# Kernel tuning notes

Hardware: AMD Instinct MI355X
Metric: run time of the kernel (lower is better)

The kernel has to match this reference:

```python
import jax, jax.numpy as jnp
import numpy as np

N = 100000
E = 1600000
EMB = 256
D = 128
B = 4096
L = 50
NCLASS = 10


def _spmm(edge_src, edge_dst, edge_w, h):
    # adj @ h with adj given as weighted edge list (dst aggregates from src)
    msg = h[edge_src] * edge_w[:, None]          # [E, D]
    return jax.ops.segment_sum(msg, edge_dst, num_segments=h.shape[0])


def setup_inputs() -> dict:
    key = jax.random.key(0)
    ks = jax.random.split(key, 20)
    inp = {}
    inp["A1_tensor"] = jax.random.normal(ks[0], (N, EMB), dtype=jnp.float32)
    inp["edge_src"] = jax.random.randint(ks[1], (E,), 0, N, dtype=jnp.int32)
    inp["edge_dst"] = jax.random.randint(ks[2], (E,), 0, N, dtype=jnp.int32)
    inp["edge_w"] = jax.random.uniform(ks[3], (E,), dtype=jnp.float32)
    inp["batch_idx"] = jax.random.randint(ks[4], (B, 1, L), 0, N, dtype=jnp.int32)
    s = 0.05  # modest init scale for numerical sanity
    inp["w_gc1"] = jax.random.normal(ks[5], (EMB, D), dtype=jnp.float32) * s
    inp["b_gc1"] = jax.random.normal(ks[6], (D,), dtype=jnp.float32) * s
    inp["w_gc2"] = jax.random.normal(ks[7], (D, D), dtype=jnp.float32) * s
    inp["b_gc2"] = jax.random.normal(ks[8], (D,), dtype=jnp.float32) * s
    inp["n_param"] = jax.random.uniform(ks[9], (N, 1), dtype=jnp.float32)
    inp["Lin1"] = jax.random.normal(ks[10], (EMB, D), dtype=jnp.float32) * s
    inp["Lin1_bias"] = jax.random.normal(ks[11], (D,), dtype=jnp.float32) * s
    inp["weight2"] = jax.random.normal(ks[12], (D, 64), dtype=jnp.float32) * s
    inp["bias2"] = jax.random.normal(ks[13], (64,), dtype=jnp.float32) * s
    inp["lin1_w"] = jax.random.normal(ks[14], ((L + 1) * 64, D), dtype=jnp.float32) * s
    inp["lin1_b"] = jax.random.normal(ks[15], (D,), dtype=jnp.float32) * s
    inp["classifier"] = jax.random.normal(ks[16], (D, NCLASS), dtype=jnp.float32) * s
    inp["classifier_bias"] = jax.random.normal(ks[17], (NCLASS,), dtype=jnp.float32) * s
    return inp


def reference(A1_tensor, edge_src, edge_dst, edge_w, batch_idx,
              w_gc1, b_gc1, w_gc2, b_gc2, n_param, Lin1, Lin1_bias,
              weight2, bias2, lin1_w, lin1_b, classifier, classifier_bias):
    # eval mode: both dropouts are identity
    a0 = A1_tensor @ Lin1 + Lin1_bias              # [N, D]
    a1 = a0 * n_param                              # per-node convex gate
    x1 = _spmm(edge_src, edge_dst, edge_w, A1_tensor @ w_gc1 + b_gc1)  # gc1
    x1 = a1 + x1 * (1.0 - n_param)
    x2 = _spmm(edge_src, edge_dst, edge_w, x1 @ w_gc2 + b_gc2)         # gc2
    bidx = batch_idx[:, 0, :]                      # [B, L]
    sel = x2[bidx]                                 # [B, L, D] irregular gather
    sel = jnp.concatenate([sel, jnp.sum(sel, axis=1, keepdims=True)], axis=1)  # [B, L+1, D]
    sel = jnp.einsum('bld,de->ble', sel, weight2) + bias2                      # [B, L+1, 64]
    sel = sel.reshape(bidx.shape[0], -1)           # [B, (L+1)*64]
    sel = sel @ lin1_w + lin1_b                    # [B, D]
    pre = sel @ classifier + classifier_bias       # [B, nclass]
    return (jnp.argmax(pre, axis=-1), sel)
```

## Files before the change

### kernel.cpp

```cpp
#include <hip/hip_runtime.h>
#include <cstdint>

#define NN   100000
#define EE   1600000
#define EMBD 256
#define DD   128
#define BBB  4096
#define LLL  50
#define NCLS 10

#define NB   196
#define BSH  9
#define EPB  4096

#define FIXS 1048576.0f
#define INVS (1.0f / 1048576.0f)

typedef __attribute__((ext_vector_type(8))) short bf16x8;
typedef __attribute__((ext_vector_type(4))) float f32x4;

__device__ __forceinline__ ushort f2bf(float f) {
  uint32_t u = __float_as_uint(f);
  u += 0x7fffu + ((u >> 16) & 1u);
  return (ushort)(u >> 16);
}
__device__ __forceinline__ float bf2f(ushort h) {
  return __uint_as_float(((uint32_t)h) << 16);
}

template<int BM, int BN, int BK, int TM, int TN>
__global__ __launch_bounds__(256)
void gemm_f32(const float* __restrict__ Av, int lda,
              const float* __restrict__ W, int ldw,
              const float* __restrict__ bias,
              float* __restrict__ Cv, int ldc,
              int M, int ktot, int kper,
              const int* __restrict__ bidxg,
              const float* __restrict__ Sg)
{
  constexpr int TX = BN / TN;
  constexpr int TY = BM / TM;
  static_assert(TX * TY == 256, "thread mapping");
  static_assert(TN % 4 == 0, "epilogue uses 4-wide vectors");
  constexpr int AQ = BK / 4;
  constexpr int ALOADS = (BM * AQ) / 256;
  static_assert((BM * AQ) % 256 == 0, "A-tile load mapping");
  constexpr int WQ4 = BN / 4;
  constexpr int WLOADS = (BK * WQ4) / 256;
  static_assert((BK * WQ4) % 256 == 0, "W-tile load mapping");

  __shared__ float As[BK][BM + 4];
  __shared__ float Ws[BK][BN];

  const int tid = threadIdx.x;
  const int tx = tid % TX, ty = tid / TX;
  const int bm0 = blockIdx.x * BM;
  const int bn0 = blockIdx.y * BN;
  const int z = blockIdx.z;
  const int koff = z * kper;
  int kc = ktot - koff; if (kc > kper) kc = kper;
  W += bn0 + (size_t)koff * ldw;
  Cv += (size_t)z * (size_t)M * ldc;
  const float* biasp = bias ? bias + bn0 : nullptr;

  float acc[TM][TN];
#pragma unroll
  for (int i = 0; i < TM; ++i)
#pragma unroll
    for (int j = 0; j < TN; ++j) acc[i][j] = 0.f;

  for (int kt = 0; kt < kc; kt += BK) {
#pragma unroll
    for (int p = 0; p < ALOADS; ++p) {
      int f = tid + p * 256;
      int row = f / AQ, q = f % AQ;
      int arow = bm0 + row;
      float4 av = make_float4(0.f, 0.f, 0.f, 0.f);
      if (arow < M) {
        if (bidxg) {
          int k = koff + kt + (q << 2);
          int l = k >> 6, jj = k & 63;
          const float* ap = (l < LLL)
              ? (Av + (size_t)bidxg[arow * LLL + l] * 64 + jj)
              : (Sg + (size_t)arow * 64 + jj);
          av = *(const float4*)ap;
        } else {
          av = *(const float4*)(Av + (long long)arow * lda + koff + kt + (q << 2));
        }
      }
      As[(q << 2) + 0][row] = av.x;
      As[(q << 2) + 1][row] = av.y;
      As[(q << 2) + 2][row] = av.z;
      As[(q << 2) + 3][row] = av.w;
    }
#pragma unroll
    for (int p = 0; p < WLOADS; ++p) {
      int f = tid + p * 256;
      int krow = f / WQ4, c4 = f % WQ4;
      *(float4*)&Ws[krow][c4 << 2] =
          *(const float4*)(W + (long long)(kt + krow) * ldw + (c4 << 2));
    }
    __syncthreads();
#pragma unroll
    for (int kk = 0; kk < BK; ++kk) {
      float a[TM], b[TN];
      if constexpr (TM % 4 == 0) {
#pragma unroll
        for (int i = 0; i < TM; i += 4)
          *(float4*)&a[i] = *(const float4*)&As[kk][ty * TM + i];
      } else {
#pragma unroll
        for (int i = 0; i < TM; ++i) a[i] = As[kk][ty * TM + i];
      }
#pragma unroll
      for (int j = 0; j < TN; j += 4)
        *(float4*)&b[j] = *(const float4*)&Ws[kk][tx * TN + j];
#pragma unroll
      for (int i = 0; i < TM; ++i)
#pragma unroll
        for (int j = 0; j < TN; ++j)
          acc[i][j] = fmaf(a[i], b[j], acc[i][j]);
    }
    __syncthreads();
  }

#pragma unroll
  for (int i = 0; i < TM; ++i) {
    int r = bm0 + ty * TM + i;
    if (r >= M) continue;
#pragma unroll
    for (int j4 = 0; j4 < TN; j4 += 4) {
      float4 v = make_float4(acc[i][j4], acc[i][j4 + 1],
                             acc[i][j4 + 2], acc[i][j4 + 3]);
      if (biasp != nullptr) {
        v.x += biasp[tx * TN + j4 + 0]; v.y += biasp[tx * TN + j4 + 1];
        v.z += biasp[tx * TN + j4 + 2]; v.w += biasp[tx * TN + j4 + 3];
      }
      *(float4*)(Cv + (long long)r * ldc + bn0 + tx * TN + j4) = v;
    }
  }
}

__global__ __launch_bounds__(256)
void gemm_qp_mfma(const float* __restrict__ A1,
                  const ushort* __restrict__ Wfh,
                  const ushort* __restrict__ Wfl,
                  const float* __restrict__ bab,
                  float* __restrict__ Qb, float* __restrict__ Pb, int M)
{
  __shared__ ushort LAh[128][40];
  __shared__ ushort LAl[128][40];
  const int tid = threadIdx.x;
  const int w = tid >> 6, l = tid & 63;
  const int bm0 = blockIdx.x * 128;
  const int srow = tid >> 1;
  const int skh = (tid & 1) << 4;
  const int fk = (l >> 4) << 3;

  f32x4 acc[2][8];
#pragma unroll
  for (int rt = 0; rt < 2; ++rt)
#pragma unroll
    for (int c = 0; c < 8; ++c) acc[rt][c] = (f32x4){0.f, 0.f, 0.f, 0.f};

  for (int kt8 = 0; kt8 < 8; ++kt8) {
    {
      int grow = bm0 + srow;
      float x[16];
      if (grow < M) {
        const float* ap = A1 + (size_t)grow * 256 + (kt8 << 5) + skh;
        *(float4*)&x[0]  = *(const float4*)ap;
        *(float4*)&x[4]  = *(const float4*)(ap + 4);
        *(float4*)&x[8]  = *(const float4*)(ap + 8);
        *(float4*)&x[12] = *(const float4*)(ap + 12);
      } else {
#pragma unroll
        for (int j = 0; j < 16; ++j) x[j] = 0.f;
      }
      ushort h[16], lo[16];
#pragma unroll
      for (int j = 0; j < 16; ++j) {
        h[j] = f2bf(x[j]);
        lo[j] = f2bf(x[j] - bf2f(h[j]));
      }
      *(bf16x8*)&LAh[srow][skh]     = *(bf16x8*)&h[0];
      *(bf16x8*)&LAh[srow][skh + 8] = *(bf16x8*)&h[8];
      *(bf16x8*)&LAl[srow][skh]     = *(bf16x8*)&lo[0];
      *(bf16x8*)&LAl[srow][skh + 8] = *(bf16x8*)&lo[8];
    }
    __syncthreads();

    bf16x8 ah[2], al[2];
#pragma unroll
    for (int rt = 0; rt < 2; ++rt) {
      int frow = (w << 5) + (rt << 4) + (l & 15);
      ah[rt] = *(const bf16x8*)&LAh[frow][fk];
      al[rt] = *(const bf16x8*)&LAl[frow][fk];
    }
#pragma unroll
    for (int ct = 0; ct < 8; ++ct) {
      size_t off = ((size_t)((kt8 << 3) + ct) * 64 + l) << 3;
      bf16x8 bh = *(const bf16x8*)(Wfh + off);
      bf16x8 bl = *(const bf16x8*)(Wfl + off);
#pragma unroll
      for (int rt = 0; rt < 2; ++rt) {
        acc[rt][ct] = __builtin_amdgcn_mfma_f32_16x16x32_bf16(ah[rt], bh, acc[rt][ct], 0, 0, 0);
        acc[rt][ct] = __builtin_amdgcn_mfma_f32_16x16x32_bf16(ah[rt], bl, acc[rt][ct], 0, 0, 0);
        acc[rt][ct] = __builtin_amdgcn_mfma_f32_16x16x32_bf16(al[rt], bh, acc[rt][ct], 0, 0, 0);
      }
    }
    __syncthreads();
  }

#pragma unroll
  for (int rt = 0; rt < 2; ++rt) {
    const int r0 = bm0 + (w << 5) + (rt << 4) + ((l >> 4) << 2);
#pragma unroll
    for (int ct = 0; ct < 8; ++ct) {
      int gcol = (ct << 4) + (l & 15);
      float bia = bab[gcol];
      float* dst = (gcol < 64) ? (Qb + gcol) : (Pb + (gcol - 64));
#pragma unroll
      for (int r = 0; r < 4; ++r) {
        int grow = r0 + r;
        if (grow < M) dst[(size_t)grow * 64] = acc[rt][ct][r] + bia;
      }
    }
  }
}

__global__ __launch_bounds__(256)
void wfrag_k(const float* __restrict__ Wab, ushort* __restrict__ Wfh,
             ushort* __restrict__ Wfl)
{
  int t = blockIdx.x * 256 + threadIdx.x;
  if (t >= 4096) return;
  int f = t >> 6, l = t & 63;
  int kt = f >> 3, ct = f & 7;
  int row0 = (kt << 5) + ((l >> 4) << 3);
  int col = (ct << 4) + (l & 15);
  ushort h[8], lo[8];
#pragma unroll
  for (int j = 0; j < 8; ++j) {
    float x = Wab[(row0 + j) * 128 + col];
    h[j] = f2bf(x);
    lo[j] = f2bf(x - bf2f(h[j]));
  }
  size_t off = ((size_t)t) << 3;
  *(bf16x8*)(Wfh + off) = *(bf16x8*)h;
  *(bf16x8*)(Wfl + off) = *(bf16x8*)lo;
}

__global__ __launch_bounds__(256)
void fuse1_k(const float* __restrict__ wgc1, const float* __restrict__ lin1,
             const float* __restrict__ bgc1, const float* __restrict__ lin1b,
             const float* __restrict__ wgc2,
             float* __restrict__ T1, float* __restrict__ T2,
             float* __restrict__ ta, float* __restrict__ tb)
{
  int t = blockIdx.x * 256 + threadIdx.x;
  const float* Arow; float* outp; int n;
  if (t < 32768)      { n = t & 127; Arow = wgc1 + (t >> 7) * 128; outp = T1 + t; }
  else if (t < 65536) { int u = t - 32768; n = u & 127; Arow = lin1 + (u >> 7) * 128; outp = T2 + u; }
  else if (t < 65664) { n = t - 65536; Arow = bgc1;  outp = ta + n; }
  else if (t < 65792) { n = t - 65664; Arow = lin1b; outp = tb + n; }
  else return;
  float s = 0.f;
  for (int k = 0; k < 128; ++k) s = fmaf(Arow[k], wgc2[k * 128 + n], s);
  *outp = s;
}

__global__ __launch_bounds__(256)
void fuse2_k(const float* __restrict__ T1, const float* __restrict__ T2,
             const float* __restrict__ ta, const float* __restrict__ tb,
             const float* __restrict__ bgc2, const float* __restrict__ w2,
             float* __restrict__ Wab, float* __restrict__ bab,
             float* __restrict__ bcv)
{
  int t = blockIdx.x * 256 + threadIdx.x;
  const float* Arow; float* outp; int j;
  if (t < 32768) {
    int c = t & 127; j = c & 63;
    Arow = (c < 64 ? T1 : T2) + (t >> 7) * 128;
    outp = Wab + t;
  } else if (t < 32896) {
    int c = t - 32768; j = c & 63; Arow = (c < 64) ? ta : tb; outp = bab + c;
  } else if (t < 32960) {
    j = t - 32896; Arow = bgc2; outp = bcv + j;
  } else return;
  float s = 0.f;
  for (int k = 0; k < 128; ++k) s = fmaf(Arow[k], w2[k * 64 + j], s);
  *outp = s;
}

__global__ __launch_bounds__(256)
void cnt_k(const int* __restrict__ edst, int* __restrict__ gbkt)
{
  __shared__ int l[NB];
  const int tid = threadIdx.x;
  for (int i = tid; i < NB; i += 256) l[i] = 0;
  __syncthreads();
  const int e0 = blockIdx.x * EPB;
  const int e1 = min(EE, e0 + EPB);
#pragma unroll
  for (int u = 0; u < 16; ++u) {
    int e = e0 + u * 256 + tid;
    if (e < e1) atomicAdd(&l[edst[e] >> BSH], 1);
  }
  __syncthreads();
  for (int i = tid; i < NB; i += 256)
    if (l[i]) atomicAdd(&gbkt[i], l[i]);
}

__global__ __launch_bounds__(256)
void scanB_k(const int* __restrict__ gbkt, int* __restrict__ bbase,
             int* __restrict__ gcur, int* __restrict__ rp)
{
  __shared__ int s[256];
  int t = threadIdx.x;
  int v = (t < NB) ? gbkt[t] : 0;
  s[t] = v;
  __syncthreads();
  for (int off = 1; off < 256; off <<= 1) {
    int u = (t >= off) ? s[t - off] : 0;
    __syncthreads();
    s[t] += u;
    __syncthreads();
  }
  if (t < NB) {
    int ex = s[t] - v;
    bbase[t] = ex;
    gcur[t] = ex;
  }
  if (t == 0) { bbase[NB] = EE; rp[NN] = EE; }
}

__global__ __launch_bounds__(256)
void bin_k(const int* __restrict__ edst, const int* __restrict__ esrc,
           const float* __restrict__ ew, int* __restrict__ gcur,
           int4* __restrict__ ebd)
{
  __shared__ int lcnt[NB];
  __shared__ int lbase[NB];
  const int tid = threadIdx.x;
  const int e0 = blockIdx.x * EPB;
  const int e1 = min(EE, e0 + EPB);
  for (int i = tid; i < NB; i += 256) lcnt[i] = 0;
  __syncthreads();
  int dv[16], sv[16], wv[16];
#pragma unroll
  for (int u = 0; u < 16; ++u) {
    int e = e0 + u * 256 + tid;
    if (e < e1) {
      dv[u] = edst[e];
      sv[u] = esrc[e];
      wv[u] = __float_as_int(ew[e]);
      atomicAdd(&lcnt[dv[u] >> BSH], 1);
    } else dv[u] = -1;
  }
  __syncthreads();
  for (int i = tid; i < NB; i += 256) {
    lbase[i] = atomicAdd(&gcur[i], lcnt[i]);
    lcnt[i] = 0;
  }
  __syncthreads();
#pragma unroll
  for (int u = 0; u < 16; ++u) {
    if (dv[u] >= 0) {
      int c = dv[u] >> BSH;
      int k = atomicAdd(&lcnt[c], 1);
      int4 p; p.x = dv[u]; p.y = sv[u]; p.z = wv[u]; p.w = 0;
      ebd[lbase[c] + k] = p;
    }
  }
}

__global__ __launch_bounds__(256)
void sort_k(const int4* __restrict__ ebd, const int* __restrict__ bbase,
            int* __restrict__ rp, int2* __restrict__ sw)
{
  __shared__ int hist[512];
  __shared__ int excl[512];
  __shared__ int s2[256];
  __shared__ int lcur[512];
  const int c = blockIdx.x;
  const int n0 = c << BSH;
  const int n1 = min(NN, n0 + 512);
  const int nn = n1 - n0;
  const int tid = threadIdx.x;
  for (int i = tid; i < 512; i += 256) { hist[i] = 0; lcur[i] = 0; }
  __syncthreads();
  const int b0 = bbase[c];
  const int b1 = bbase[c + 1];
  for (int i = b0 + tid; i < b1; i += 256)
    atomicAdd(&hist[ebd[i].x - n0], 1);
  __syncthreads();
  int a0 = hist[2 * tid], a1 = hist[2 * tid + 1];
  s2[tid] = a0 + a1;
  __syncthreads();
  for (int off = 1; off < 256; off <<= 1) {
    int u = (tid >= off) ? s2[tid - off] : 0;
    __syncthreads();
    s2[tid] += u;
    __syncthreads();
  }
  int pe = tid ? s2[tid - 1] : 0;
  excl[2 * tid] = pe;
  excl[2 * tid + 1] = pe + a0;
  if (2 * tid < nn)     rp[n0 + 2 * tid]     = b0 + pe;
  if (2 * tid + 1 < nn) rp[n0 + 2 * tid + 1] = b0 + pe + a0;
  __syncthreads();
  for (int i = b0 + tid; i < b1; i += 256) {
    int4 p = ebd[i];
    int li = p.x - n0;
    int k = atomicAdd(&lcur[li], 1);
    int2 q; q.x = p.y; q.y = p.z;
    sw[b0 + excl[li] + k] = q;
  }
}

template<int MODE>
__global__ __launch_bounds__(256)
void spmm64(const int* __restrict__ rp, const int2* __restrict__ sw,
            const float* __restrict__ Gf, float* __restrict__ xout,
            const float* __restrict__ bias, const float* __restrict__ npar,
            const float* __restrict__ Pb)
{
  int widx = blockIdx.x * 4 + (threadIdx.x >> 6);
  if (widx >= NN) return;
  int lane = threadIdx.x & 63;
  int e0 = rp[widx], e1 = rp[widx + 1];
  int acc = 0;
  int j = e0;
  for (; j + 8 <= e1; j += 8) {
    float gv[8], wv[8];
#pragma unroll
    for (int u = 0; u < 8; ++u) {
      int2 q = sw[j + u];
      wv[u] = __int_as_float(q.y);
      gv[u] = Gf[(size_t)q.x * 64 + lane];
    }
#pragma unroll
    for (int u = 0; u < 8; ++u)
      acc += __float2int_rn(gv[u] * wv[u] * FIXS);
  }
  for (; j < e1; ++j) {
    int2 q = sw[j];
    acc += __float2int_rn(Gf[(size_t)q.x * 64 + lane] *
                          __int_as_float(q.y) * FIXS);
  }
  float v = (float)acc * INVS;
  if (MODE == 1) {
    xout[(size_t)widx * 64 + lane] = v + bias[lane];
  } else {
    float nv = npar[widx];
    float p = Pb[(size_t)widx * 64 + lane];
    xout[(size_t)widx * 64 + lane] = nv * p + (1.f - nv) * v + bias[lane];
  }
}

__global__ __launch_bounds__(256)
void sumS_k(const float* __restrict__ Z, const int* __restrict__ bidx,
            const float* __restrict__ b2, float* __restrict__ S)
{
  int wv = threadIdx.x >> 6;
  int lane = threadIdx.x & 63;
  int b = blockIdx.x * 4 + wv;
  if (b >= BBB) return;
  const int* bi = bidx + (size_t)b * LLL;
  float s = 0.f;
  for (int l = 0; l < LLL; ++l)
    s += Z[(size_t)bi[l] * 64 + lane];
  S[(size_t)b * 64 + lane] = s - 49.f * b2[lane];
}

__global__ __launch_bounds__(256)
void reduce8_k(const float* __restrict__ P8, const float* __restrict__ l1b,
               float* __restrict__ sel)
{
  int t = blockIdx.x * 256 + threadIdx.x;
  if (t >= BBB * 32) return;
  int r = t >> 5, c4 = t & 31;
  size_t off = (size_t)r * 128 + (c4 << 2);
  const size_t zs = (size_t)BBB * 128;
  float4 o = *(const float4*)(P8 + off);
#pragma unroll
  for (int z = 1; z < 8; ++z) {
    float4 s = *(const float4*)(P8 + z * zs + off);
    o.x += s.x; o.y += s.y; o.z += s.z; o.w += s.w;
  }
  float4 b = *(const float4*)(l1b + (c4 << 2));
  o.x += b.x; o.y += b.y; o.z += b.z; o.w += b.w;
  *(float4*)(sel + off) = o;
}

__global__ __launch_bounds__(256)
void cls_k(const float* __restrict__ sel, const float* __restrict__ Wc,
           const float* __restrict__ bc, float* __restrict__ outIdx)
{
  int wv = threadIdx.x >> 6;
  int lane = threadIdx.x & 63;
  int b = blockIdx.x * 4 + wv;
  if (b >= BBB) return;
  float logit = -1e30f;
  if (lane < NCLS) {
    float s = bc[lane];
    const float* sr = sel + (size_t)b * DD;
    for (int d = 0; d < DD; ++d) s = fmaf(sr[d], Wc[d * NCLS + lane], s);
    logit = s;
  }
  float best = -1e30f; int bi = 0;
  for (int c = 0; c < NCLS; ++c) {
    float v = __shfl(logit, c, 64);
    if (v > best) { best = v; bi = c; }
  }
  if (lane == 0) outIdx[b] = (float)bi;
}

extern "C" void kernel_launch(void* const* d_in, const int* in_sizes, int n_in,
                              void* d_out, int out_size, void* d_ws, size_t ws_size,
                              hipStream_t stream)
{
  const float* A1    = (const float*)d_in[0];
  const int*   esrc  = (const int*)d_in[1];
  const int*   edst  = (const int*)d_in[2];
  const float* ew    = (const float*)d_in[3];
  const int*   bidx  = (const int*)d_in[4];
  const float* wgc1  = (const float*)d_in[5];
  const float* bgc1  = (const float*)d_in[6];
  const float* wgc2  = (const float*)d_in[7];
  const float* bgc2  = (const float*)d_in[8];
  const float* npar  = (const float*)d_in[9];
  const float* lin1  = (const float*)d_in[10];
  const float* lin1b = (const float*)d_in[11];
  const float* w2    = (const float*)d_in[12];
  const float* b2    = (const float*)d_in[13];
  const float* l1w   = (const float*)d_in[14];
  const float* l1b   = (const float*)d_in[15];
  const float* clsw  = (const float*)d_in[16];
  const float* clsb  = (const float*)d_in[17];

  float* out = (float*)d_out;
  float* sel = out + BBB;

  uint8_t* ws   = (uint8_t*)d_ws;
  int4*    ebd  = (int4*) (ws);
  float*   Qb   = (float*)(ws);
  float*   Z    = (float*)(ws);
  float*   Pb   = (float*)(ws + 25600000);
  float*   G    = (float*)(ws + 51200000);
  float*   P8   = (float*)(ws + 51200000);
  int2*    sw   = (int2*) (ws + 76800000);
  int*     rp   = (int*)  (ws + 89600000);
  int*     gbkt = (int*)  (ws + 90000016);
  int*     gcur = (int*)  (ws + 90001040);
  int*     bbase= (int*)  (ws + 90002064);
  float*   S    = (float*)(ws + 90400528);
  float*   T1   = (float*)(ws + 91449104);
  float*   T2   = (float*)(ws + 91580176);
  float*   Wab  = (float*)(ws + 91711248);
  float*   ta   = (float*)(ws + 91842320);
  float*   tb   = (float*)(ws + 91842832);
  float*   bab  = (float*)(ws + 91843344);
  float*   bcv  = (float*)(ws + 91843856);
  ushort*  Wfh  = (ushort*)(ws + 91844112);
  ushort*  Wfl  = (ushort*)(ws + 91909648);

  dim3 blk(256);
  const int gEB = (EE + EPB - 1) / EPB;

  hipLaunchKernelGGL(fuse1_k, dim3(257), blk, 0, stream,
      wgc1, lin1, bgc1, lin1b, wgc2, T1, T2, ta, tb);
  hipLaunchKernelGGL(fuse2_k, dim3(129), blk, 0, stream,
      T1, T2, ta, tb, bgc2, w2, Wab, bab, bcv);
  hipLaunchKernelGGL(wfrag_k, dim3(16), blk, 0, stream, Wab, Wfh, Wfl);

  hipMemsetAsync(gbkt, 0, NB * 4, stream);
  hipLaunchKernelGGL(cnt_k, dim3(gEB), blk, 0, stream, edst, gbkt);
  hipLaunchKernelGGL(scanB_k, dim3(1), blk, 0, stream, gbkt, bbase, gcur, rp);
  hipLaunchKernelGGL(bin_k, dim3(gEB), blk, 0, stream, edst, esrc, ew, gcur, ebd);
  hipLaunchKernelGGL(sort_k, dim3(NB), blk, 0, stream, ebd, bbase, rp, sw);

  hipLaunchKernelGGL(gemm_qp_mfma, dim3((NN + 127) / 128), blk, 0, stream,
      A1, Wfh, Wfl, bab, Qb, Pb, NN);

  hipLaunchKernelGGL((spmm64<2>), dim3(NN / 4), blk, 0, stream,
      rp, sw, Qb, G, bcv, npar, Pb);

  hipLaunchKernelGGL((spmm64<1>), dim3(NN / 4), blk, 0, stream,
      rp, sw, G, Z, b2, (const float*)nullptr, (const float*)nullptr);

  hipLaunchKernelGGL(sumS_k, dim3(BBB / 4), blk, 0, stream, Z, bidx, b2, S);

  hipLaunchKernelGGL((gemm_f32<64,64,32,4,4>), dim3(BBB / 64, 2, 8), blk, 0, stream,
      Z, 64, l1w, DD, (const float*)nullptr, P8, DD,
      BBB, (LLL + 1) * 64, 13 * 32, bidx, S);

  hipLaunchKernelGGL(reduce8_k, dim3(BBB * 32 / 256), blk, 0, stream, P8, l1b, sel);

  hipLaunchKernelGGL(cls_k, dim3(BBB / 4), blk, 0, stream, sel, clsw, clsb, out);
}
```

Before: 370.5 us.

## Double-buffer GEMM A tiles with register prefetch and split binned edge arrays

The QP GEMM now double-buffers its LDS A tiles and prefetches the next K-slice of A1 into registers while the current slice's MFMAs run. This removes one barrier per iteration and overlaps global loads with compute. Separately, the binning step now writes destination indices and (src, weight) pairs as separate int/int2 arrays instead of padded int4 records. This cuts write and read bytes in bin_k and sort_k, and lets the histogram pass read only the destination array. The costs are twice the LDS per GEMM block and extra register pressure.

```diff
diff --git a/kernel.cpp b/kernel.cpp
--- a/kernel.cpp
+++ b/kernel.cpp
@@ -148,14 +148,17 @@
                   const float* __restrict__ bab,
                   float* __restrict__ Qb, float* __restrict__ Pb, int M)
 {
-  __shared__ ushort LAh[128][40];
-  __shared__ ushort LAl[128][40];
+  __shared__ ushort LAh[2][128][40];
+  __shared__ ushort LAl[2][128][40];
   const int tid = threadIdx.x;
   const int w = tid >> 6, l = tid & 63;
   const int bm0 = blockIdx.x * 128;
   const int srow = tid >> 1;
   const int skh = (tid & 1) << 4;
   const int fk = (l >> 4) << 3;
+  const int grow = bm0 + srow;
+  const bool rok = grow < M;
+  const float* aptr = A1 + (size_t)grow * 256 + skh;
 
   f32x4 acc[2][8];
 #pragma unroll
@@ -163,39 +166,46 @@
 #pragma unroll
     for (int c = 0; c < 8; ++c) acc[rt][c] = (f32x4){0.f, 0.f, 0.f, 0.f};
 
+  float x[16];
+#pragma unroll
+  for (int j = 0; j < 16; ++j) x[j] = 0.f;
+  if (rok) {
+    *(float4*)&x[0]  = *(const float4*)(aptr + 0);
+    *(float4*)&x[4]  = *(const float4*)(aptr + 4);
+    *(float4*)&x[8]  = *(const float4*)(aptr + 8);
+    *(float4*)&x[12] = *(const float4*)(aptr + 12);
+  }
+
   for (int kt8 = 0; kt8 < 8; ++kt8) {
+    const int buf = kt8 & 1;
     {
-      int grow = bm0 + srow;
-      float x[16];
-      if (grow < M) {
-        const float* ap = A1 + (size_t)grow * 256 + (kt8 << 5) + skh;
-        *(float4*)&x[0]  = *(const float4*)ap;
-        *(float4*)&x[4]  = *(const float4*)(ap + 4);
-        *(float4*)&x[8]  = *(const float4*)(ap + 8);
-        *(float4*)&x[12] = *(const float4*)(ap + 12);
-      } else {
-#pragma unroll
-        for (int j = 0; j < 16; ++j) x[j] = 0.f;
-      }
       ushort h[16], lo[16];
 #pragma unroll
       for (int j = 0; j < 16; ++j) {
         h[j] = f2bf(x[j]);
         lo[j] = f2bf(x[j] - bf2f(h[j]));
       }
-      *(bf16x8*)&LAh[srow][skh]     = *(bf16x8*)&h[0];
-      *(bf16x8*)&LAh[srow][skh + 8] = *(bf16x8*)&h[8];
-      *(bf16x8*)&LAl[srow][skh]     = *(bf16x8*)&lo[0];
-      *(bf16x8*)&LAl[srow][skh + 8] = *(bf16x8*)&lo[8];
+      *(bf16x8*)&LAh[buf][srow][skh]     = *(bf16x8*)&h[0];
+      *(bf16x8*)&LAh[buf][srow][skh + 8] = *(bf16x8*)&h[8];
+      *(bf16x8*)&LAl[buf][srow][skh]     = *(bf16x8*)&lo[0];
+      *(bf16x8*)&LAl[buf][srow][skh + 8] = *(bf16x8*)&lo[8];
     }
     __syncthreads();
+
+    if (kt8 < 7 && rok) {
+      const float* ap = aptr + ((kt8 + 1) << 5);
+      *(float4*)&x[0]  = *(const float4*)(ap + 0);
+      *(float4*)&x[4]  = *(const float4*)(ap + 4);
+      *(float4*)&x[8]  = *(const float4*)(ap + 8);
+      *(float4*)&x[12] = *(const float4*)(ap + 12);
+    }
 
     bf16x8 ah[2], al[2];
 #pragma unroll
     for (int rt = 0; rt < 2; ++rt) {
       int frow = (w << 5) + (rt << 4) + (l & 15);
-      ah[rt] = *(const bf16x8*)&LAh[frow][fk];
-      al[rt] = *(const bf16x8*)&LAl[frow][fk];
+      ah[rt] = *(const bf16x8*)&LAh[buf][frow][fk];
+      al[rt] = *(const bf16x8*)&LAl[buf][frow][fk];
     }
 #pragma unroll
     for (int ct = 0; ct < 8; ++ct) {
@@ -209,7 +219,6 @@
         acc[rt][ct] = __builtin_amdgcn_mfma_f32_16x16x32_bf16(al[rt], bh, acc[rt][ct], 0, 0, 0);
       }
     }
-    __syncthreads();
   }
 
 #pragma unroll
@@ -222,8 +231,8 @@
       float* dst = (gcol < 64) ? (Qb + gcol) : (Pb + (gcol - 64));
 #pragma unroll
       for (int r = 0; r < 4; ++r) {
-        int grow = r0 + r;
-        if (grow < M) dst[(size_t)grow * 64] = acc[rt][ct][r] + bia;
+        int grw = r0 + r;
+        if (grw < M) dst[(size_t)grw * 64] = acc[rt][ct][r] + bia;
       }
     }
   }
@@ -338,7 +347,7 @@
 __global__ __launch_bounds__(256)
 void bin_k(const int* __restrict__ edst, const int* __restrict__ esrc,
            const float* __restrict__ ew, int* __restrict__ gcur,
-           int4* __restrict__ ebd)
+           int2* __restrict__ ebs, int* __restrict__ ebdd)
 {
   __shared__ int lcnt[NB];
   __shared__ int lbase[NB];
@@ -369,14 +378,17 @@
     if (dv[u] >= 0) {
       int c = dv[u] >> BSH;
       int k = atomicAdd(&lcnt[c], 1);
-      int4 p; p.x = dv[u]; p.y = sv[u]; p.z = wv[u]; p.w = 0;
-      ebd[lbase[c] + k] = p;
-    }
-  }
-}
-
-__global__ __launch_bounds__(256)
-void sort_k(const int4* __restrict__ ebd, const int* __restrict__ bbase,
+      int pos = lbase[c] + k;
+      int2 q; q.x = sv[u]; q.y = wv[u];
+      ebs[pos] = q;
+      ebdd[pos] = dv[u];
+    }
+  }
+}
+
+__global__ __launch_bounds__(256)
+void sort_k(const int2* __restrict__ ebs, const int* __restrict__ ebdd,
+            const int* __restrict__ bbase,
             int* __restrict__ rp, int2* __restrict__ sw)
 {
   __shared__ int hist[512];
@@ -393,7 +405,7 @@
   const int b0 = bbase[c];
   const int b1 = bbase[c + 1];
   for (int i = b0 + tid; i < b1; i += 256)
-    atomicAdd(&hist[ebd[i].x - n0], 1);
+    atomicAdd(&hist[ebdd[i] - n0], 1);
   __syncthreads();
   int a0 = hist[2 * tid], a1 = hist[2 * tid + 1];
   s2[tid] = a0 + a1;
@@ -411,11 +423,9 @@
   if (2 * tid + 1 < nn) rp[n0 + 2 * tid + 1] = b0 + pe + a0;
   __syncthreads();
   for (int i = b0 + tid; i < b1; i += 256) {
-    int4 p = ebd[i];
-    int li = p.x - n0;
+    int li = ebdd[i] - n0;
     int k = atomicAdd(&lcur[li], 1);
-    int2 q; q.x = p.y; q.y = p.z;
-    sw[b0 + excl[li] + k] = q;
+    sw[b0 + excl[li] + k] = ebs[i];
   }
 }
 
@@ -544,7 +554,8 @@
   float* sel = out + BBB;
 
   uint8_t* ws   = (uint8_t*)d_ws;
-  int4*    ebd  = (int4*) (ws);
+  int2*    ebs  = (int2*) (ws);
+  int*     ebdd = (int*)  (ws + 12800000);
   float*   Qb   = (float*)(ws);
   float*   Z    = (float*)(ws);
   float*   Pb   = (float*)(ws + 25600000);
@@ -578,8 +589,9 @@
   hipMemsetAsync(gbkt, 0, NB * 4, stream);
   hipLaunchKernelGGL(cnt_k, dim3(gEB), blk, 0, stream, edst, gbkt);
   hipLaunchKernelGGL(scanB_k, dim3(1), blk, 0, stream, gbkt, bbase, gcur, rp);
-  hipLaunchKernelGGL(bin_k, dim3(gEB), blk, 0, stream, edst, esrc, ew, gcur, ebd);
-  hipLaunchKernelGGL(sort_k, dim3(NB), blk, 0, stream, ebd, bbase, rp, sw);
+  hipLaunchKernelGGL(bin_k, dim3(gEB), blk, 0, stream, edst, esrc, ew, gcur,
+      ebs, ebdd);
+  hipLaunchKernelGGL(sort_k, dim3(NB), blk, 0, stream, ebs, ebdd, bbase, rp, sw);
 
   hipLaunchKernelGGL(gemm_qp_mfma, dim3((NN + 127) / 128), blk, 0, stream,
       A1, Wfh, Wfl, bab, Qb, Pb, NN);
```

Result: slower. 384.3 us (+3.7%).
